# Performance work log

Measured on AMD Instinct MI355X. Metric: run time of the kernel, lower is better.

Reference implementation:

```python
import jax, jax.numpy as jnp
import numpy as np
import math

FANO_LINES = [(0,1,2),(0,3,4),(0,6,5),(1,3,5),(1,4,6),(2,3,6),(2,5,4)]
WINDOW = 16

def fano_mask(T: int) -> jnp.ndarray:
    """[7,T,T] bool mask: head h attends to j if (j%7 in line_h and j<=i) or i-WINDOW<=j<=i."""
    membership = np.zeros((7, 7), dtype=bool)
    for h, line in enumerate(FANO_LINES):
        membership[h, list(line)] = True
    j = np.arange(T)
    fano = membership[:, j % 7]                      # [7,T]
    i = j[:, None]
    causal = (j[None, :] <= i)                       # [T,T]
    local = causal & (j[None, :] >= i - WINDOW)      # [T,T]
    mask = (fano[:, None, :] & causal[None]) | local[None]
    return jnp.asarray(mask)

def setup_inputs() -> dict:
    key = jax.random.key(0)
    ks = jax.random.split(key, 5)
    B, T, D = 1, 4096, 896
    s = 1.0 / math.sqrt(D)
    return {
        "x":  jax.random.normal(ks[0], (B, T, D), dtype=jnp.float32),
        "Wq": jax.random.normal(ks[1], (D, D), dtype=jnp.float32) * s,
        "Wk": jax.random.normal(ks[2], (D, D), dtype=jnp.float32) * s,
        "Wv": jax.random.normal(ks[3], (D, D), dtype=jnp.float32) * s,
        "Wo": jax.random.normal(ks[4], (D, D), dtype=jnp.float32) * s,
    }

def reference(x, Wq, Wk, Wv, Wo):
    B, T, D = x.shape
    H = 7
    hd = D // H
    # torch Linear: x @ W.T
    q = (x @ Wq.T).reshape(B, T, H, hd)
    k = (x @ Wk.T).reshape(B, T, H, hd)
    v = (x @ Wv.T).reshape(B, T, H, hd)
    scale = 1.0 / math.sqrt(hd)
    scores = jnp.einsum('bthc,bshc->bhts', q, k) * scale   # [B,7,T,T]
    mask = fano_mask(T)                                    # [7,T,T]
    neg = jnp.asarray(-jnp.inf, dtype=scores.dtype)
    scores = jnp.where(mask[None], scores, neg)
    attn = jax.nn.softmax(scores, axis=-1)
    out = jnp.einsum('bhts,bshc->bthc', attn, v).reshape(B, T, D)
    return out @ Wo.T
```

## Files before the change

### kernel.cpp

```cpp
#include <hip/hip_runtime.h>
#include <stdint.h>

typedef unsigned short ushort_t;
typedef __bf16 bf16x8 __attribute__((ext_vector_type(8)));
typedef __bf16 bf16x2 __attribute__((ext_vector_type(2)));
typedef float f32x4 __attribute__((ext_vector_type(4)));

#define T_SEQ 4096
#define D_MODEL 896
#define CHUNKS_PER_BLOCK 4
#define MAXSPLIT 8

#define LSK 136
#define LSV 72

__constant__ int d_LINEMASK[7] = {0x07, 0x19, 0x61, 0x2A, 0x52, 0x4C, 0x34};
__constant__ int d_R[7][3] = {{0,1,2},{0,3,4},{0,5,6},{1,3,5},{1,4,6},{2,3,6},{2,4,5}};

__device__ inline unsigned f2bf(float f) {
    unsigned x = __float_as_uint(f);
    return (x + 0x7fffu + ((x >> 16) & 1u)) >> 16;
}
__device__ inline float lo_f(unsigned x) { return __uint_as_float(x << 16); }
__device__ inline float hi_f(unsigned x) { return __uint_as_float(x & 0xFFFF0000u); }

__device__ __forceinline__ unsigned pk_bf2(float lo, float hi) {
    union { bf16x2 h; unsigned u; } cv;
    cv.h = (bf16x2){(__bf16)lo, (__bf16)hi};
    return cv.u;
}
__device__ __forceinline__ ushort_t bf1(float f) {
    union { __bf16 h; ushort_t u; } cv;
    cv.h = (__bf16)f;
    return cv.u;
}

__host__ __device__ inline int nsplit_of(int t) {
    int a = (192 * t + 189) / 7 + 3;
    int nch_ub = (a + 63) >> 6;
    return (nch_ub + 2 + CHUNKS_PER_BLOCK - 1) / CHUNKS_PER_BLOCK;
}

__global__ __launch_bounds__(256)
void cvt5(const float* __restrict__ x,  const float* __restrict__ wq,
          const float* __restrict__ wk, const float* __restrict__ wv,
          const float* __restrict__ wo,
          ushort_t* __restrict__ xb,  ushort_t* __restrict__ wqb,
          ushort_t* __restrict__ wkb, ushort_t* __restrict__ wvb,
          ushort_t* __restrict__ wob) {
    const int ten = blockIdx.y;
    const float* s = (ten == 0) ? x : (ten == 1) ? wq : (ten == 2) ? wk
                   : (ten == 3) ? wv : wo;
    ushort_t* d = (ten == 0) ? xb : (ten == 1) ? wqb : (ten == 2) ? wkb
                : (ten == 3) ? wvb : wob;
    const int n8 = ((ten == 0) ? T_SEQ * D_MODEL : D_MODEL * D_MODEL) >> 3;
    for (int i = blockIdx.x * 256 + threadIdx.x; i < n8; i += gridDim.x * 256) {
        float4 a = ((const float4*)s)[2 * i];
        float4 b = ((const float4*)s)[2 * i + 1];
        uint4 u;
        u.x = f2bf(a.x) | (f2bf(a.y) << 16);
        u.y = f2bf(a.z) | (f2bf(a.w) << 16);
        u.z = f2bf(b.x) | (f2bf(b.y) << 16);
        u.w = f2bf(b.z) | (f2bf(b.w) << 16);
        ((uint4*)d)[i] = u;
    }
}

__device__ __forceinline__ void async_cp16(const void* g, void* l) {
    __builtin_amdgcn_global_load_lds(
        (__attribute__((address_space(1))) void*)g,
        (__attribute__((address_space(3))) void*)l,
        16, 0, 0);
}

template <bool C32>
__global__ __launch_bounds__(256)
void gemm_nt_dma(const ushort_t* __restrict__ A,
                 const ushort_t* __restrict__ B0,
                 const ushort_t* __restrict__ B1,
                 const ushort_t* __restrict__ B2,
                 void* __restrict__ C0,
                 void* __restrict__ C1,
                 void* __restrict__ C2) {
    const int z = blockIdx.z;
    const ushort_t* B = (z == 0) ? B0 : (z == 1) ? B1 : B2;
    void* C = (z == 0) ? C0 : (z == 1) ? C1 : C2;

    const int K = D_MODEL, N = D_MODEL;
    const int i0 = blockIdx.x * 128;
    const int n0 = blockIdx.y * 128;

    __shared__ __align__(16) ushort_t As[128 * 32];
    __shared__ __align__(16) ushort_t Bs[128 * 32];

    const int t = threadIdx.x;
    const int w = t >> 6, lane = t & 63;
    const int wm = (w >> 1) * 64, wn = (w & 1) * 64;
    const int lr = lane & 15, lq = lane >> 4;

    const int srow = w * 16 + (lane >> 2);
    const int scol = (lane & 3) * 8;
    const ushort_t* gA0 = A + (size_t)(i0 + srow) * K + scol;
    const ushort_t* gA1 = A + (size_t)(i0 + 64 + srow) * K + scol;
    const ushort_t* gB0 = B + (size_t)(n0 + srow) * K + scol;
    const ushort_t* gB1 = B + (size_t)(n0 + 64 + srow) * K + scol;
    ushort_t* lA0 = &As[(w * 16) * 32];
    ushort_t* lA1 = &As[(64 + w * 16) * 32];
    ushort_t* lB0 = &Bs[(w * 16) * 32];
    ushort_t* lB1 = &Bs[(64 + w * 16) * 32];

    f32x4 acc[4][4];
#pragma unroll
    for (int a = 0; a < 4; a++)
#pragma unroll
        for (int b = 0; b < 4; b++) acc[a][b] = (f32x4){0.f, 0.f, 0.f, 0.f};

    for (int k0 = 0; k0 < K; k0 += 32) {
        __syncthreads();
        async_cp16(gA0 + k0, lA0);
        async_cp16(gA1 + k0, lA1);
        async_cp16(gB0 + k0, lB0);
        async_cp16(gB1 + k0, lB1);
        __builtin_amdgcn_s_waitcnt(0);
        __syncthreads();

        bf16x8 af[4], bfr[4];
#pragma unroll
        for (int mi = 0; mi < 4; mi++)
            af[mi] = *(const bf16x8*)&As[(wm + mi * 16 + lr) * 32 + lq * 8];
#pragma unroll
        for (int ni = 0; ni < 4; ni++)
            bfr[ni] = *(const bf16x8*)&Bs[(wn + ni * 16 + lr) * 32 + lq * 8];
#pragma unroll
        for (int mi = 0; mi < 4; mi++)
#pragma unroll
            for (int ni = 0; ni < 4; ni++)
                acc[mi][ni] = __builtin_amdgcn_mfma_f32_16x16x32_bf16(
                    af[mi], bfr[ni], acc[mi][ni], 0, 0, 0);
    }

    if (C32) {
        float* Cf = (float*)C;
#pragma unroll
        for (int mi = 0; mi < 4; mi++)
#pragma unroll
            for (int ni = 0; ni < 4; ni++)
#pragma unroll
                for (int r = 0; r < 4; r++) {
                    int row = i0 + wm + mi * 16 + lq * 4 + r;
                    int col = n0 + wn + ni * 16 + lr;
                    Cf[(size_t)row * N + col] = acc[mi][ni][r];
                }
    } else {
        ushort_t* Cb = (ushort_t*)C;
#pragma unroll
        for (int mi = 0; mi < 4; mi++)
#pragma unroll
            for (int ni = 0; ni < 4; ni++)
#pragma unroll
                for (int r = 0; r < 4; r++) {
                    int row = i0 + wm + mi * 16 + lq * 4 + r;
                    int col = n0 + wn + ni * 16 + lr;
                    Cb[(size_t)row * N + col] = (ushort_t)f2bf(acc[mi][ni][r]);
                }
    }
}

__device__ inline void vt_scatter8(ushort_t* vtcol, uint4 vv) {
    vtcol[0 * LSV] = (ushort_t)(vv.x & 0xFFFFu);
    vtcol[1 * LSV] = (ushort_t)(vv.x >> 16);
    vtcol[2 * LSV] = (ushort_t)(vv.y & 0xFFFFu);
    vtcol[3 * LSV] = (ushort_t)(vv.y >> 16);
    vtcol[4 * LSV] = (ushort_t)(vv.z & 0xFFFFu);
    vtcol[5 * LSV] = (ushort_t)(vv.z >> 16);
    vtcol[6 * LSV] = (ushort_t)(vv.w & 0xFFFFu);
    vtcol[7 * LSV] = (ushort_t)(vv.w >> 16);
}

__device__ inline int jof(int p, int r0, int r1, int r2) {
    int g = p / 3, rs = p - 3 * g;
    return 7 * g + ((rs == 0) ? r0 : (rs == 1) ? r1 : r2);
}

__device__ __forceinline__ void issue_kv(const ushort_t* __restrict__ Kb,
                                         const ushort_t* __restrict__ Vb,
                                         int j, int h, int dim0,
                                         uint4 kreg[4], uint4 vreg[4]) {
    if (j >= 0 && j < T_SEQ) {
        const ushort_t* kp = Kb + (size_t)j * D_MODEL + h * 128 + dim0;
        const ushort_t* vp = Vb + (size_t)j * D_MODEL + h * 128 + dim0;
#pragma unroll
        for (int v = 0; v < 4; v++) {
            kreg[v] = *(const uint4*)(kp + v * 8);
            vreg[v] = *(const uint4*)(vp + v * 8);
        }
    } else {
        uint4 zz = {0u, 0u, 0u, 0u};
#pragma unroll
        for (int v = 0; v < 4; v++) { kreg[v] = zz; vreg[v] = zz; }
    }
}

__device__ __forceinline__ void write_kv(ushort_t* Ks, ushort_t* Vt,
                                         int kk, int dim0,
                                         const uint4 kreg[4], const uint4 vreg[4]) {
#pragma unroll
    for (int v = 0; v < 4; v++) {
        *(uint4*)&Ks[kk * LSK + dim0 + v * 8] = kreg[v];
        vt_scatter8(&Vt[(dim0 + v * 8) * LSV + kk], vreg[v]);
    }
}

__global__ __launch_bounds__(256, 3)
void fano_attn_split(const ushort_t* __restrict__ Qb,
                     const ushort_t* __restrict__ Kb,
                     const ushort_t* __restrict__ Vb,
                     ushort_t* __restrict__ Opart,
                     float* __restrict__ Lm) {
    const int h = blockIdx.y;
    const int p = (int)gridDim.x - 1 - (int)blockIdx.x;

    int tile = 63, pbase0 = 0;
    for (int u = 0; u < 64; ++u) {
        int s = nsplit_of(u);
        if (p < pbase0 + s) { tile = u; break; }
        pbase0 += s;
    }
    const int sp = p - pbase0;
    const int Sloc = nsplit_of(tile);

    const int i0 = tile * 64;
    const int t = threadIdx.x;
    const int w = t >> 6, lane = t & 63;
    const int lr = lane & 15, quad = lane >> 4;
    const int iw0 = i0 + w * 16;

    __shared__ __align__(16) ushort_t Ks[64 * LSK];
    __shared__ __align__(16) ushort_t Vt[128 * LSV];

    const int lm = d_LINEMASK[h];
    const int r0 = d_R[h][0], r1 = d_R[h][1], r2 = d_R[h][2];
    const float scale = 0.08838834764831845f;

    bf16x8 qf[4];
    {
        const ushort_t* qrow = Qb + (size_t)(iw0 + lr) * D_MODEL + h * 128;
#pragma unroll
        for (int f = 0; f < 4; f++)
            qf[f] = *(const bf16x8*)(qrow + f * 32 + quad * 8);
    }

    f32x4 O[8];
#pragma unroll
    for (int dt = 0; dt < 8; dt++) O[dt] = (f32x4){0.f, 0.f, 0.f, 0.f};
    float m = -1e30f;
    float l = 0.f;

    const int imax = i0 + 63;
    const int ncomp = (imax - r0) / 7 + (imax - r1) / 7 + (imax - r2) / 7 + 3;
    const int nch = (ncomp + 63) >> 6;
    const int ntot = nch + 2;
    const int cstart = (sp * ntot) / Sloc;
    const int cend = ((sp + 1) * ntot) / Sloc;

    auto chunk_j = [&](int cc) -> int {
        if (cc >= nch) {
            const int jbase = (cc == nch) ? i0 - 16 : i0 + 48;
            return jbase + lane;
        }
        return jof(cc * 64 + lane, r0, r1, r2);
    };

    uint4 kreg[4], vreg[4];
    if (cstart < cend)
        issue_kv(Kb, Vb, chunk_j(cstart), h, w * 32, kreg, vreg);

    const int iq = iw0 + lr;

    for (int cc = cstart; cc < cend; cc++) {
        const bool band = (cc >= nch);
        const int jbase = (cc == nch) ? i0 - 16 : i0 + 48;

        __syncthreads();
        write_kv(Ks, Vt, lane, w * 32, kreg, vreg);
        __syncthreads();

        if (cc + 1 < cend)
            issue_kv(Kb, Vb, chunk_j(cc + 1), h, w * 32, kreg, vreg);

        {
            int jmin = band ? jbase : jof(cc * 64, r0, r1, r2);
            if (jmin > iw0 + 15) continue;
        }

        f32x4 S[4];
#pragma unroll
        for (int tn = 0; tn < 4; tn++) S[tn] = (f32x4){0.f, 0.f, 0.f, 0.f};
#pragma unroll
        for (int f = 0; f < 4; f++) {
            bf16x8 kf[4];
#pragma unroll
            for (int tn = 0; tn < 4; tn++)
                kf[tn] = *(const bf16x8*)&Ks[(tn * 16 + lr) * LSK + f * 32 + quad * 8];
#pragma unroll
            for (int tn = 0; tn < 4; tn++)
                S[tn] = __builtin_amdgcn_mfma_f32_16x16x32_bf16(kf[tn], qf[f], S[tn], 0, 0, 0);
        }

        const bool interior = !band && (jof(cc * 64 + 63, r0, r1, r2) <= iw0);
        if (interior) {
#pragma unroll
            for (int tn = 0; tn < 4; tn++)
#pragma unroll
                for (int r = 0; r < 4; r++) S[tn][r] *= scale;
        } else if (band) {
#pragma unroll
            for (int tn = 0; tn < 4; tn++)
#pragma unroll
                for (int r = 0; r < 4; r++) {
                    int j = jbase + tn * 16 + quad * 4 + r;
                    int jm = ((j % 7) + 7) % 7;
                    bool ok = (j >= 0) && !((lm >> jm) & 1) &&
                              (j <= iq) && (j >= iq - 16);
                    S[tn][r] = ok ? S[tn][r] * scale : -1e30f;
                }
        } else {
#pragma unroll
            for (int tn = 0; tn < 4; tn++) {
                int p0 = cc * 64 + tn * 16 + quad * 4;
                int g = p0 / 3, rs = p0 - 3 * g;
#pragma unroll
                for (int r = 0; r < 4; r++) {
                    int j = 7 * g + ((rs == 0) ? r0 : (rs == 1) ? r1 : r2);
                    S[tn][r] = (j <= iq) ? S[tn][r] * scale : -1e30f;
                    if (++rs == 3) { rs = 0; ++g; }
                }
            }
        }

        float cm = -1e30f;
#pragma unroll
        for (int tn = 0; tn < 4; tn++)
#pragma unroll
            for (int r = 0; r < 4; r++) cm = fmaxf(cm, S[tn][r]);
        cm = fmaxf(cm, __shfl_xor(cm, 16));
        cm = fmaxf(cm, __shfl_xor(cm, 32));

        const bool defer = __all(cm <= m && m >= -60.f);
        float mn, a = 1.f;
        if (defer) {
            mn = m;
        } else {
            mn = fmaxf(fmaxf(m, cm), -60.f);
            a = __expf(m - mn);
            m = mn;
        }
        float pr[4][4];
        float rs_ = 0.f;
#pragma unroll
        for (int tn = 0; tn < 4; tn++)
#pragma unroll
            for (int r = 0; r < 4; r++) {
                pr[tn][r] = __expf(S[tn][r] - mn);
                rs_ += pr[tn][r];
            }
        rs_ += __shfl_xor(rs_, 16);
        rs_ += __shfl_xor(rs_, 32);
        if (defer) {
            l = l + rs_;
        } else {
            l = l * a + rs_;
            float a4[4];
#pragma unroll
            for (int r = 0; r < 4; r++) a4[r] = __shfl(a, quad * 4 + r);
#pragma unroll
            for (int dt = 0; dt < 8; dt++)
#pragma unroll
                for (int r = 0; r < 4; r++) O[dt][r] *= a4[r];
        }

        unsigned u01[4], u23[4];
#pragma unroll
        for (int tn = 0; tn < 4; tn++) {
            u01[tn] = pk_bf2(pr[tn][0], pr[tn][1]);
            u23[tn] = pk_bf2(pr[tn][2], pr[tn][3]);
        }
        const int srcA = 32 * (quad & 1) + lr;
        const int srcB = srcA + 16;
        const bool hi = (quad >= 2);
        uint4 t0, t1;
        {
            unsigned d0a = __shfl(u01[0], srcA), d0b = __shfl(u01[1], srcA);
            unsigned d1a = __shfl(u23[0], srcA), d1b = __shfl(u23[1], srcA);
            unsigned d2a = __shfl(u01[0], srcB), d2b = __shfl(u01[1], srcB);
            unsigned d3a = __shfl(u23[0], srcB), d3b = __shfl(u23[1], srcB);
            t0.x = hi ? d0b : d0a;
            t0.y = hi ? d1b : d1a;
            t0.z = hi ? d2b : d2a;
            t0.w = hi ? d3b : d3a;
        }
        {
            unsigned d0a = __shfl(u01[2], srcA), d0b = __shfl(u01[3], srcA);
            unsigned d1a = __shfl(u23[2], srcA), d1b = __shfl(u23[3], srcA);
            unsigned d2a = __shfl(u01[2], srcB), d2b = __shfl(u01[3], srcB);
            unsigned d3a = __shfl(u23[2], srcB), d3b = __shfl(u23[3], srcB);
            t1.x = hi ? d0b : d0a;
            t1.y = hi ? d1b : d1a;
            t1.z = hi ? d2b : d2a;
            t1.w = hi ? d3b : d3a;
        }
        bf16x8 pf0 = *(const bf16x8*)&t0;
        bf16x8 pf1 = *(const bf16x8*)&t1;

#pragma unroll
        for (int dt = 0; dt < 8; dt++) {
            bf16x8 v0 = *(const bf16x8*)&Vt[(dt * 16 + lr) * LSV + quad * 8];
            bf16x8 v1 = *(const bf16x8*)&Vt[(dt * 16 + lr) * LSV + 32 + quad * 8];
            O[dt] = __builtin_amdgcn_mfma_f32_16x16x32_bf16(pf0, v0, O[dt], 0, 0, 0);
            O[dt] = __builtin_amdgcn_mfma_f32_16x16x32_bf16(pf1, v1, O[dt], 0, 0, 0);
        }
    }

    const size_t pbase = ((size_t)p * 7 + h) * 64;
#pragma unroll
    for (int dt = 0; dt < 8; dt++)
#pragma unroll
        for (int r = 0; r < 4; r++) {
            int lrow = w * 16 + quad * 4 + r;
            Opart[(pbase + lrow) * 128 + dt * 16 + lr] = bf1(O[dt][r]);
        }
    if (quad == 0) {
        int lrow = w * 16 + lr;
        Lm[(pbase + lrow) * 2 + 0] = m;
        Lm[(pbase + lrow) * 2 + 1] = l;
    }
}

__global__ __launch_bounds__(256)
void attn_merge(const ushort_t* __restrict__ Opart,
                const float* __restrict__ Lm,
                ushort_t* __restrict__ Ab) {
    const int h = blockIdx.y;
    const int tt = blockIdx.x;
    int pb = 0;
    for (int u = 0; u < tt; ++u) pb += nsplit_of(u);
    const int S = nsplit_of(tt);
    const int lrow = threadIdx.x >> 2;
    const int row = tt * 64 + lrow;
    const int d0 = (threadIdx.x & 3) * 32;

    float ms[MAXSPLIT], ls[MAXSPLIT], M = -1e30f;
#pragma unroll
    for (int s = 0; s < MAXSPLIT; s++) {
        ms[s] = -1e30f;
        ls[s] = 0.f;
        if (s < S) {
            size_t q = (((size_t)(pb + s) * 7 + h) * 64 + lrow) * 2;
            ms[s] = Lm[q];
            ls[s] = Lm[q + 1];
        }
        M = fmaxf(M, ms[s]);
    }
    float L = 0.f, c[MAXSPLIT];
#pragma unroll
    for (int s = 0; s < MAXSPLIT; s++) {
        c[s] = __expf(ms[s] - M);
        L += c[s] * ls[s];
    }
    float acc[32];
#pragma unroll
    for (int k = 0; k < 32; k++) acc[k] = 0.f;
#pragma unroll
    for (int s = 0; s < MAXSPLIT; s++) {
        if (s < S) {
            const float cs = c[s];
            const ushort_t* op =
                Opart + (((size_t)(pb + s) * 7 + h) * 64 + lrow) * 128 + d0;
#pragma unroll
            for (int v = 0; v < 4; v++) {
                uint4 u = *(const uint4*)(op + v * 8);
                acc[v * 8 + 0] += cs * lo_f(u.x);
                acc[v * 8 + 1] += cs * hi_f(u.x);
                acc[v * 8 + 2] += cs * lo_f(u.y);
                acc[v * 8 + 3] += cs * hi_f(u.y);
                acc[v * 8 + 4] += cs * lo_f(u.z);
                acc[v * 8 + 5] += cs * hi_f(u.z);
                acc[v * 8 + 6] += cs * lo_f(u.w);
                acc[v * 8 + 7] += cs * hi_f(u.w);
            }
        }
    }
    float invL = 1.f / L;
    ushort_t* dst = Ab + (size_t)row * D_MODEL + h * 128 + d0;
#pragma unroll
    for (int v = 0; v < 4; v++) {
        uint4 u;
        u.x = f2bf(acc[v * 8 + 0] * invL) | (f2bf(acc[v * 8 + 1] * invL) << 16);
        u.y = f2bf(acc[v * 8 + 2] * invL) | (f2bf(acc[v * 8 + 3] * invL) << 16);
        u.z = f2bf(acc[v * 8 + 4] * invL) | (f2bf(acc[v * 8 + 5] * invL) << 16);
        u.w = f2bf(acc[v * 8 + 6] * invL) | (f2bf(acc[v * 8 + 7] * invL) << 16);
        *(uint4*)(dst + v * 8) = u;
    }
}

extern "C" void kernel_launch(void* const* d_in, const int* in_sizes, int n_in,
                              void* d_out, int out_size, void* d_ws, size_t ws_size,
                              hipStream_t stream) {
    const float* x  = (const float*)d_in[0];
    const float* Wq = (const float*)d_in[1];
    const float* Wk = (const float*)d_in[2];
    const float* Wv = (const float*)d_in[3];
    const float* Wo = (const float*)d_in[4];

    int NP = 0;
    for (int u = 0; u < 64; ++u) NP += nsplit_of(u);

    const size_t n  = (size_t)T_SEQ * D_MODEL;
    const size_t nw = (size_t)D_MODEL * D_MODEL;
    ushort_t* xb  = (ushort_t*)d_ws + 128;
    ushort_t* Wqb = xb + n;
    ushort_t* Wkb = Wqb + nw;
    ushort_t* Wvb = Wkb + nw;
    ushort_t* Wob = Wvb + nw;
    ushort_t* Qb  = Wob + nw;
    ushort_t* Kb  = Qb + n;
    ushort_t* Vb  = Kb + n;
    ushort_t* Ab  = Vb + n;
    ushort_t* Opart = Ab + n;
    float*    Lm  = (float*)(Opart + (size_t)NP * 7 * 64 * 128);

    cvt5<<<dim3(1792, 5), 256, 0, stream>>>(x, Wq, Wk, Wv, Wo,
                                            xb, Wqb, Wkb, Wvb, Wob);
    gemm_nt_dma<false><<<dim3(32, 7, 3), 256, 0, stream>>>(
        xb, Wqb, Wkb, Wvb, Qb, Kb, Vb);
    fano_attn_split<<<dim3(NP, 7), 256, 0, stream>>>(
        Qb, Kb, Vb, Opart, Lm);
    attn_merge<<<dim3(64, 7), 256, 0, stream>>>(Opart, Lm, Ab);
    gemm_nt_dma<true><<<dim3(32, 7, 1), 256, 0, stream>>>(
        Ab, Wob, Wob, Wob, d_out, d_out, d_out);
}
```

Before: 130.7 us.

## Switch attention to 32x32 MFMA tiles with split-K warps and double-buffered LDS

Rewrites the attention inner loop to use 32x32x16 bf16 MFMAs. Each wave handles a 32-query by 32-key sub-tile, and the two key-halves are merged through shared memory at the end. K/V staging becomes double-buffered with a two-deep register prefetch, so there is one barrier per chunk instead of two. The softmax P-fragment shuffle is simplified to a single xor-32 exchange. Occupancy drops from 3 to 2 blocks per CU because of the larger LDS and register footprint, and an extra cross-wave merge is added.

```diff
diff --git a/kernel.cpp b/kernel.cpp
--- a/kernel.cpp
+++ b/kernel.cpp
@@ -5,6 +5,7 @@
 typedef __bf16 bf16x8 __attribute__((ext_vector_type(8)));
 typedef __bf16 bf16x2 __attribute__((ext_vector_type(2)));
 typedef float f32x4 __attribute__((ext_vector_type(4)));
+typedef float f32x16 __attribute__((ext_vector_type(16)));
 
 #define T_SEQ 4096
 #define D_MODEL 896
@@ -27,11 +28,6 @@
 __device__ __forceinline__ unsigned pk_bf2(float lo, float hi) {
     union { bf16x2 h; unsigned u; } cv;
     cv.h = (bf16x2){(__bf16)lo, (__bf16)hi};
-    return cv.u;
-}
-__device__ __forceinline__ ushort_t bf1(float f) {
-    union { __bf16 h; ushort_t u; } cv;
-    cv.h = (__bf16)f;
     return cv.u;
 }
 
@@ -211,7 +207,7 @@
     }
 }
 
-__global__ __launch_bounds__(256, 3)
+__global__ __launch_bounds__(256, 2)
 void fano_attn_split(const ushort_t* __restrict__ Qb,
                      const ushort_t* __restrict__ Kb,
                      const ushort_t* __restrict__ Vb,
@@ -232,27 +228,31 @@
     const int i0 = tile * 64;
     const int t = threadIdx.x;
     const int w = t >> 6, lane = t & 63;
-    const int lr = lane & 15, quad = lane >> 4;
-    const int iw0 = i0 + w * 16;
-
-    __shared__ __align__(16) ushort_t Ks[64 * LSK];
-    __shared__ __align__(16) ushort_t Vt[128 * LSV];
+    const int wq = w >> 1, wk = w & 1;
+    const int q = lane & 31;
+    const int hl = lane >> 5;
+    const int iq = i0 + wq * 32 + q;
+
+    __shared__ __align__(16) ushort_t Ks[2][64 * LSK];
+    __shared__ __align__(16) ushort_t Vt[2][128 * LSV];
 
     const int lm = d_LINEMASK[h];
     const int r0 = d_R[h][0], r1 = d_R[h][1], r2 = d_R[h][2];
     const float scale = 0.08838834764831845f;
 
-    bf16x8 qf[4];
+    bf16x8 qf[8];
     {
-        const ushort_t* qrow = Qb + (size_t)(iw0 + lr) * D_MODEL + h * 128;
-#pragma unroll
-        for (int f = 0; f < 4; f++)
-            qf[f] = *(const bf16x8*)(qrow + f * 32 + quad * 8);
-    }
-
-    f32x4 O[8];
-#pragma unroll
-    for (int dt = 0; dt < 8; dt++) O[dt] = (f32x4){0.f, 0.f, 0.f, 0.f};
+        const ushort_t* qrow = Qb + (size_t)iq * D_MODEL + h * 128;
+#pragma unroll
+        for (int f = 0; f < 8; f++)
+            qf[f] = *(const bf16x8*)(qrow + f * 16 + hl * 8);
+    }
+
+    f32x16 O[4];
+#pragma unroll
+    for (int d4 = 0; d4 < 4; d4++)
+#pragma unroll
+        for (int e = 0; e < 16; e++) O[d4][e] = 0.f;
     float m = -1e30f;
     float l = 0.f;
 
@@ -272,167 +272,182 @@
     };
 
     uint4 kreg[4], vreg[4];
-    if (cstart < cend)
+    if (cstart < cend) {
         issue_kv(Kb, Vb, chunk_j(cstart), h, w * 32, kreg, vreg);
-
-    const int iq = iw0 + lr;
+        write_kv(Ks[0], Vt[0], lane, w * 32, kreg, vreg);
+        if (cstart + 1 < cend)
+            issue_kv(Kb, Vb, chunk_j(cstart + 1), h, w * 32, kreg, vreg);
+    }
+    __syncthreads();
+    int cur = 0;
 
     for (int cc = cstart; cc < cend; cc++) {
         const bool band = (cc >= nch);
         const int jbase = (cc == nch) ? i0 - 16 : i0 + 48;
 
+        if (cc + 1 < cend)
+            write_kv(Ks[cur ^ 1], Vt[cur ^ 1], lane, w * 32, kreg, vreg);
+        if (cc + 2 < cend)
+            issue_kv(Kb, Vb, chunk_j(cc + 2), h, w * 32, kreg, vreg);
+
+        int jmin = band ? jbase : jof(cc * 64, r0, r1, r2);
+        if (jmin <= i0 + wq * 32 + 31) {
+            const ushort_t* KsC = Ks[cur];
+            const ushort_t* VtC = Vt[cur];
+
+            f32x16 S;
+#pragma unroll
+            for (int e = 0; e < 16; e++) S[e] = 0.f;
+#pragma unroll
+            for (int f = 0; f < 8; f++) {
+                bf16x8 kf = *(const bf16x8*)
+                    &KsC[(wk * 32 + q) * LSK + f * 16 + hl * 8];
+                S = __builtin_amdgcn_mfma_f32_32x32x16_bf16(kf, qf[f], S, 0, 0, 0);
+            }
+
+            const bool interior = !band && (jof(cc * 64 + 63, r0, r1, r2) <= i0 + wq * 32);
+            if (interior) {
+#pragma unroll
+                for (int e = 0; e < 16; e++) S[e] *= scale;
+            } else if (band) {
+#pragma unroll
+                for (int g4 = 0; g4 < 4; g4++) {
+                    int j0 = jbase + wk * 32 + 8 * g4 + 4 * hl;
+#pragma unroll
+                    for (int e = 0; e < 4; e++) {
+                        int j = j0 + e;
+                        int jm = ((j % 7) + 7) % 7;
+                        bool ok = (j >= 0) && !((lm >> jm) & 1) &&
+                                  (j <= iq) && (j >= iq - 16);
+                        S[g4 * 4 + e] = ok ? S[g4 * 4 + e] * scale : -1e30f;
+                    }
+                }
+            } else {
+#pragma unroll
+                for (int g4 = 0; g4 < 4; g4++) {
+                    int p0 = cc * 64 + wk * 32 + 8 * g4 + 4 * hl;
+                    int g = p0 / 3, rs = p0 - 3 * g;
+#pragma unroll
+                    for (int e = 0; e < 4; e++) {
+                        int j = 7 * g + ((rs == 0) ? r0 : (rs == 1) ? r1 : r2);
+                        S[g4 * 4 + e] = (j <= iq) ? S[g4 * 4 + e] * scale : -1e30f;
+                        if (++rs == 3) { rs = 0; ++g; }
+                    }
+                }
+            }
+
+            float cm = -1e30f;
+#pragma unroll
+            for (int e = 0; e < 16; e++) cm = fmaxf(cm, S[e]);
+            cm = fmaxf(cm, __shfl_xor(cm, 32));
+
+            const bool defer = __all(cm <= m && m >= -60.f);
+            float mn, a = 1.f;
+            if (defer) {
+                mn = m;
+            } else {
+                mn = fmaxf(fmaxf(m, cm), -60.f);
+                a = __expf(m - mn);
+                m = mn;
+            }
+            float rs_ = 0.f;
+#pragma unroll
+            for (int e = 0; e < 16; e++) {
+                S[e] = __expf(S[e] - mn);
+                rs_ += S[e];
+            }
+            rs_ += __shfl_xor(rs_, 32);
+            if (defer) {
+                l = l + rs_;
+            } else {
+                l = l * a + rs_;
+#pragma unroll
+                for (int d4 = 0; d4 < 4; d4++)
+#pragma unroll
+                    for (int e = 0; e < 16; e++) O[d4][e] *= a;
+            }
+
+            bf16x8 pf[2];
+#pragma unroll
+            for (int f = 0; f < 2; f++) {
+                unsigned lo0 = pk_bf2(S[8 * f + 0], S[8 * f + 1]);
+                unsigned lo1 = pk_bf2(S[8 * f + 2], S[8 * f + 3]);
+                unsigned hi0 = pk_bf2(S[8 * f + 4], S[8 * f + 5]);
+                unsigned hi1 = pk_bf2(S[8 * f + 6], S[8 * f + 7]);
+                unsigned s0 = hl ? lo0 : hi0;
+                unsigned s1 = hl ? lo1 : hi1;
+                unsigned rv0 = __shfl_xor(s0, 32);
+                unsigned rv1 = __shfl_xor(s1, 32);
+                uint4 tw;
+                tw.x = hl ? rv0 : lo0;
+                tw.y = hl ? rv1 : lo1;
+                tw.z = hl ? hi0 : rv0;
+                tw.w = hl ? hi1 : rv1;
+                pf[f] = *(const bf16x8*)&tw;
+            }
+
+#pragma unroll
+            for (int d4 = 0; d4 < 4; d4++) {
+#pragma unroll
+                for (int f = 0; f < 2; f++) {
+                    bf16x8 vf = *(const bf16x8*)
+                        &VtC[(d4 * 32 + q) * LSV + wk * 32 + f * 16 + hl * 8];
+                    O[d4] = __builtin_amdgcn_mfma_f32_32x32x16_bf16(vf, pf[f], O[d4], 0, 0, 0);
+                }
+            }
+        }
+
         __syncthreads();
-        write_kv(Ks, Vt, lane, w * 32, kreg, vreg);
-        __syncthreads();
-
-        if (cc + 1 < cend)
-            issue_kv(Kb, Vb, chunk_j(cc + 1), h, w * 32, kreg, vreg);
-
-        {
-            int jmin = band ? jbase : jof(cc * 64, r0, r1, r2);
-            if (jmin > iw0 + 15) continue;
-        }
-
-        f32x4 S[4];
-#pragma unroll
-        for (int tn = 0; tn < 4; tn++) S[tn] = (f32x4){0.f, 0.f, 0.f, 0.f};
-#pragma unroll
-        for (int f = 0; f < 4; f++) {
-            bf16x8 kf[4];
-#pragma unroll
-            for (int tn = 0; tn < 4; tn++)
-                kf[tn] = *(const bf16x8*)&Ks[(tn * 16 + lr) * LSK + f * 32 + quad * 8];
-#pragma unroll
-            for (int tn = 0; tn < 4; tn++)
-                S[tn] = __builtin_amdgcn_mfma_f32_16x16x32_bf16(kf[tn], qf[f], S[tn], 0, 0, 0);
-        }
-
-        const bool interior = !band && (jof(cc * 64 + 63, r0, r1, r2) <= iw0);
-        if (interior) {
-#pragma unroll
-            for (int tn = 0; tn < 4; tn++)
-#pragma unroll
-                for (int r = 0; r < 4; r++) S[tn][r] *= scale;
-        } else if (band) {
-#pragma unroll
-            for (int tn = 0; tn < 4; tn++)
-#pragma unroll
-                for (int r = 0; r < 4; r++) {
-                    int j = jbase + tn * 16 + quad * 4 + r;
-                    int jm = ((j % 7) + 7) % 7;
-                    bool ok = (j >= 0) && !((lm >> jm) & 1) &&
-                              (j <= iq) && (j >= iq - 16);
-                    S[tn][r] = ok ? S[tn][r] * scale : -1e30f;
+        cur ^= 1;
+    }
+
+    float* sc = (float*)&Ks[0][0];
+    float* mlsc = (float*)&Vt[0][0];
+    if (wk == 1) {
+#pragma unroll
+        for (int d4 = 0; d4 < 4; d4++)
+#pragma unroll
+            for (int e = 0; e < 16; e++) {
+                int d = d4 * 32 + (e & 3) + 8 * (e >> 2) + 4 * hl;
+                sc[((size_t)wq * 128 + d) * 32 + q] = O[d4][e];
+            }
+        if (hl == 0) {
+            mlsc[(wq * 32 + q) * 2 + 0] = m;
+            mlsc[(wq * 32 + q) * 2 + 1] = l;
+        }
+    }
+    __syncthreads();
+    if (wk == 0) {
+        float m1 = mlsc[(wq * 32 + q) * 2 + 0];
+        float l1 = mlsc[(wq * 32 + q) * 2 + 1];
+        float mm = fmaxf(m, m1);
+        float a0 = __expf(m - mm), a1 = __expf(m1 - mm);
+        float lL = l * a0 + l1 * a1;
+
+        const size_t pbase = ((size_t)p * 7 + h) * 64;
+        const int row = wq * 32 + q;
+#pragma unroll
+        for (int d4 = 0; d4 < 4; d4++)
+#pragma unroll
+            for (int rg = 0; rg < 4; rg++) {
+                float v0_, v1_, v2_, v3_;
+                {
+                    int e = rg * 4;
+                    int dA = d4 * 32 + 8 * rg + 4 * hl;
+                    v0_ = O[d4][e + 0] * a0 + sc[((size_t)wq * 128 + dA + 0) * 32 + q] * a1;
+                    v1_ = O[d4][e + 1] * a0 + sc[((size_t)wq * 128 + dA + 1) * 32 + q] * a1;
+                    v2_ = O[d4][e + 2] * a0 + sc[((size_t)wq * 128 + dA + 2) * 32 + q] * a1;
+                    v3_ = O[d4][e + 3] * a0 + sc[((size_t)wq * 128 + dA + 3) * 32 + q] * a1;
                 }
-        } else {
-#pragma unroll
-            for (int tn = 0; tn < 4; tn++) {
-                int p0 = cc * 64 + tn * 16 + quad * 4;
-                int g = p0 / 3, rs = p0 - 3 * g;
-#pragma unroll
-                for (int r = 0; r < 4; r++) {
-                    int j = 7 * g + ((rs == 0) ? r0 : (rs == 1) ? r1 : r2);
-                    S[tn][r] = (j <= iq) ? S[tn][r] * scale : -1e30f;
-                    if (++rs == 3) { rs = 0; ++g; }
-                }
-            }
-        }
-
-        float cm = -1e30f;
-#pragma unroll
-        for (int tn = 0; tn < 4; tn++)
-#pragma unroll
-            for (int r = 0; r < 4; r++) cm = fmaxf(cm, S[tn][r]);
-        cm = fmaxf(cm, __shfl_xor(cm, 16));
-        cm = fmaxf(cm, __shfl_xor(cm, 32));
-
-        const bool defer = __all(cm <= m && m >= -60.f);
-        float mn, a = 1.f;
-        if (defer) {
-            mn = m;
-        } else {
-            mn = fmaxf(fmaxf(m, cm), -60.f);
-            a = __expf(m - mn);
-            m = mn;
-        }
-        float pr[4][4];
-        float rs_ = 0.f;
-#pragma unroll
-        for (int tn = 0; tn < 4; tn++)
-#pragma unroll
-            for (int r = 0; r < 4; r++) {
-                pr[tn][r] = __expf(S[tn][r] - mn);
-                rs_ += pr[tn][r];
-            }
-        rs_ += __shfl_xor(rs_, 16);
-        rs_ += __shfl_xor(rs_, 32);
-        if (defer) {
-            l = l + rs_;
-        } else {
-            l = l * a + rs_;
-            float a4[4];
-#pragma unroll
-            for (int r = 0; r < 4; r++) a4[r] = __shfl(a, quad * 4 + r);
-#pragma unroll
-            for (int dt = 0; dt < 8; dt++)
-#pragma unroll
-                for (int r = 0; r < 4; r++) O[dt][r] *= a4[r];
-        }
-
-        unsigned u01[4], u23[4];
-#pragma unroll
-        for (int tn = 0; tn < 4; tn++) {
-            u01[tn] = pk_bf2(pr[tn][0], pr[tn][1]);
-            u23[tn] = pk_bf2(pr[tn][2], pr[tn][3]);
-        }
-        const int srcA = 32 * (quad & 1) + lr;
-        const int srcB = srcA + 16;
-        const bool hi = (quad >= 2);
-        uint4 t0, t1;
-        {
-            unsigned d0a = __shfl(u01[0], srcA), d0b = __shfl(u01[1], srcA);
-            unsigned d1a = __shfl(u23[0], srcA), d1b = __shfl(u23[1], srcA);
-            unsigned d2a = __shfl(u01[0], srcB), d2b = __shfl(u01[1], srcB);
-            unsigned d3a = __shfl(u23[0], srcB), d3b = __shfl(u23[1], srcB);
-            t0.x = hi ? d0b : d0a;
-            t0.y = hi ? d1b : d1a;
-            t0.z = hi ? d2b : d2a;
-            t0.w = hi ? d3b : d3a;
-        }
-        {
-            unsigned d0a = __shfl(u01[2], srcA), d0b = __shfl(u01[3], srcA);
-            unsigned d1a = __shfl(u23[2], srcA), d1b = __shfl(u23[3], srcA);
-            unsigned d2a = __shfl(u01[2], srcB), d2b = __shfl(u01[3], srcB);
-            unsigned d3a = __shfl(u23[2], srcB), d3b = __shfl(u23[3], srcB);
-            t1.x = hi ? d0b : d0a;
-            t1.y = hi ? d1b : d1a;
-            t1.z = hi ? d2b : d2a;
-            t1.w = hi ? d3b : d3a;
-        }
-        bf16x8 pf0 = *(const bf16x8*)&t0;
-        bf16x8 pf1 = *(const bf16x8*)&t1;
-
-#pragma unroll
-        for (int dt = 0; dt < 8; dt++) {
-            bf16x8 v0 = *(const bf16x8*)&Vt[(dt * 16 + lr) * LSV + quad * 8];
-            bf16x8 v1 = *(const bf16x8*)&Vt[(dt * 16 + lr) * LSV + 32 + quad * 8];
-            O[dt] = __builtin_amdgcn_mfma_f32_16x16x32_bf16(pf0, v0, O[dt], 0, 0, 0);
-            O[dt] = __builtin_amdgcn_mfma_f32_16x16x32_bf16(pf1, v1, O[dt], 0, 0, 0);
-        }
-    }
-
-    const size_t pbase = ((size_t)p * 7 + h) * 64;
-#pragma unroll
-    for (int dt = 0; dt < 8; dt++)
-#pragma unroll
-        for (int r = 0; r < 4; r++) {
-            int lrow = w * 16 + quad * 4 + r;
-            Opart[(pbase + lrow) * 128 + dt * 16 + lr] = bf1(O[dt][r]);
-        }
-    if (quad == 0) {
-        int lrow = w * 16 + lr;
-        Lm[(pbase + lrow) * 2 + 0] = m;
-        Lm[(pbase + lrow) * 2 + 1] = l;
+                uint2 u;
+                u.x = pk_bf2(v0_, v1_);
+                u.y = pk_bf2(v2_, v3_);
+                *(uint2*)&Opart[(pbase + row) * 128 + d4 * 32 + 8 * rg + 4 * hl] = u;
+            }
+        if (hl == 0) {
+            Lm[(pbase + row) * 2 + 0] = mm;
+            Lm[(pbase + row) * 2 + 1] = lL;
+        }
     }
 }
 
```

Result: slower. 147.1 us (+12.6%).
